# Optimization experiments

Hardware: AMD Instinct MI355X
Metric: run time of the kernel (lower is better)

## Reference

```python
import jax, jax.numpy as jnp
import numpy as np

N_NODES = 50000
N_EDGES = 800000
D_FEAT = 96


def setup_inputs() -> dict:
    key = jax.random.key(0)
    kx, ks, kd = jax.random.split(key, 3)
    x = jax.random.normal(kx, (N_NODES, D_FEAT), dtype=jnp.float32)
    src = jax.random.randint(ks, (N_EDGES,), 0, N_NODES, dtype=jnp.int64)
    dst = jax.random.randint(kd, (N_EDGES,), 0, N_NODES, dtype=jnp.int64)
    return {"x": x, "src": src, "dst": dst}


def reference(x, src, dst):
    n = x.shape[0]
    ones = jnp.ones(src.shape[0], dtype=x.dtype)
    # out-degree: edges leaving each node (src side)
    out_deg = jnp.clip(jax.ops.segment_sum(ones, src, num_segments=n), 1.0, None)
    # in-degree: edges arriving at each node (dst side)
    in_deg = jnp.clip(jax.ops.segment_sum(ones, dst, num_segments=n), 1.0, None)
    # pre-scale by out-degree^{-1/2}
    xs = x * (out_deg ** -0.5)[:, None]
    # copy_u + sum aggregation: sum messages from src into dst
    agg = jax.ops.segment_sum(xs[src], dst, num_segments=n)
    # post-scale by in-degree^{-1/2}
    return agg * (in_deg ** -0.5)[:, None]
```

## Files before the change

### kernel.cpp

```cpp
#include <hip/hip_runtime.h>


#define D_FEAT 96
#define CAP 64
#define PART_SHIFT 8
#define PNODES 256
#define NP_MAX 256
#define EPB 4096
#define OVF_CAP 8192

__device__ __forceinline__ unsigned short f2bf_rne(float f) {
    unsigned u = __float_as_uint(f);
    unsigned r = (u >> 16) & 1u;
    u += 0x7fffu + r;
    return (unsigned short)(u >> 16);
}


__global__ __launch_bounds__(256) void partition_kernel(
        const int* __restrict__ src, const int* __restrict__ dst,
        int n_edges, int np, int stride,
        int* __restrict__ pcur_d, int* __restrict__ pcur_s,
        unsigned* __restrict__ pbuf_d, unsigned short* __restrict__ pbuf_s,
        int* __restrict__ ctr,
        int* __restrict__ povf_d, int* __restrict__ sovf_d) {
    __shared__ int hcd[NP_MAX], hcs[NP_MAX];
    __shared__ int bd[NP_MAX], bs_[NP_MAX];
    __shared__ int od[NP_MAX], os_[NP_MAX];
    const int base = blockIdx.x * EPB;

    for (int i = threadIdx.x; i < NP_MAX; i += 256) {
        hcd[i] = 0; hcs[i] = 0; od[i] = 0; os_[i] = 0;
    }
    __syncthreads();

    unsigned v[16];
    #pragma unroll
    for (int k = 0; k < 16; ++k) {
        int i = base + (int)threadIdx.x + (k << 8);
        if (i < n_edges) {
            int s = src[i], d = dst[i];
            unsigned pv = (unsigned)d | ((unsigned)s << 16);
            v[k] = pv;
            atomicAdd(&hcd[d >> PART_SHIFT], 1);
            atomicAdd(&hcs[s >> PART_SHIFT], 1);
        }
    }
    __syncthreads();

    for (int p = threadIdx.x; p < np; p += 256) {
        int cd = hcd[p];
        bd[p] = cd ? atomicAdd(&pcur_d[p], cd) : 0;
        int cs = hcs[p];
        bs_[p] = cs ? atomicAdd(&pcur_s[p], cs) : 0;
    }
    __syncthreads();

    #pragma unroll
    for (int k = 0; k < 16; ++k) {
        int i = base + (int)threadIdx.x + (k << 8);
        if (i < n_edges) {
            unsigned pv = v[k];
            int d = (int)(pv & 0xffffu);
            int s = (int)(pv >> 16);
            int pd = d >> PART_SHIFT;
            int j = bd[pd] + atomicAdd(&od[pd], 1);
            if (j < stride) pbuf_d[(size_t)pd * stride + j] = pv;
            else { int k2 = atomicAdd(&ctr[1], 1); if (k2 < OVF_CAP) povf_d[k2] = (int)pv; }
            int ps = s >> PART_SHIFT;
            int j2 = bs_[ps] + atomicAdd(&os_[ps], 1);
            if (j2 < stride) pbuf_s[(size_t)ps * stride + j2] = (unsigned short)s;
            else { int k3 = atomicAdd(&ctr[2], 1); if (k3 < OVF_CAP) sovf_d[k3] = s; }
        }
    }
}


__global__ __launch_bounds__(256) void bin2_kernel(
        const unsigned* __restrict__ pbuf_d, const int* __restrict__ pcur_d,
        int stride, int n_nodes,
        int* __restrict__ cursor, unsigned short* __restrict__ slots,
        int* __restrict__ ctr, int* __restrict__ ovf_d) {
    __shared__ unsigned short lslots[PNODES * CAP];
    __shared__ int lcnt[PNODES];
    const int b = blockIdx.x;
    const int nbase = b << PART_SHIFT;
    const int nloc = min(PNODES, n_nodes - nbase);

    for (int i = threadIdx.x; i < PNODES; i += 256) lcnt[i] = 0;
    __syncthreads();

    int n = pcur_d[b]; if (n > stride) n = stride;
    for (int i = threadIdx.x; i < n; i += 256) {
        unsigned pv = pbuf_d[(size_t)b * stride + i];
        int dl = (int)(pv & 0xffu);
        int s  = (int)(pv >> 16);
        int pos = atomicAdd(&lcnt[dl], 1);
        if (pos < CAP) lslots[dl * CAP + pos] = (unsigned short)s;
        else { int k = atomicAdd(&ctr[0], 1); if (k < OVF_CAP) ovf_d[k] = (int)pv; }
    }
    __syncthreads();

    for (int i = threadIdx.x; i < nloc; i += 256) cursor[nbase + i] = lcnt[i];
    const unsigned* ls = (const unsigned*)lslots;
    unsigned* gs = (unsigned*)slots + (size_t)nbase * (CAP / 2);
    const int ncopy = nloc * (CAP / 2);
    for (int i = threadIdx.x; i < ncopy; i += 256) gs[i] = ls[i];
}


__global__ __launch_bounds__(256) void cnt2_kernel(
        const unsigned short* __restrict__ pbuf_s, const int* __restrict__ pcur_s,
        int stride, int n_nodes, int* __restrict__ out_cnt) {
    __shared__ int lcnt[PNODES];
    const int b = blockIdx.x;
    const int nbase = b << PART_SHIFT;
    const int nloc = min(PNODES, n_nodes - nbase);

    for (int i = threadIdx.x; i < PNODES; i += 256) lcnt[i] = 0;
    __syncthreads();

    int n = pcur_s[b]; if (n > stride) n = stride;
    for (int i = threadIdx.x; i < n; i += 256) {
        int s = (int)pbuf_s[(size_t)b * stride + i];
        atomicAdd(&lcnt[s & (PNODES - 1)], 1);
    }
    __syncthreads();

    for (int i = threadIdx.x; i < nloc; i += 256) out_cnt[nbase + i] = lcnt[i];
}

__global__ void fixup_kernel(int* __restrict__ ctr,
                             const int* __restrict__ povf_d,
                             const int* __restrict__ sovf_d,
                             int* __restrict__ ovf_d,
                             int* __restrict__ cursor,
                             int* __restrict__ out_cnt) {
    int np_ = ctr[1]; if (np_ > OVF_CAP) np_ = OVF_CAP;
    for (int i = threadIdx.x; i < np_; i += 256) {
        unsigned pv = (unsigned)povf_d[i];
        atomicAdd(&cursor[pv & 0xffffu], 1);
        int k = atomicAdd(&ctr[0], 1);
        if (k < OVF_CAP) ovf_d[k] = (int)pv;
    }
    int ns_ = ctr[2]; if (ns_ > OVF_CAP) ns_ = OVF_CAP;
    for (int i = threadIdx.x; i < ns_; i += 256)
        atomicAdd(&out_cnt[(unsigned)sovf_d[i]], 1);
}


__global__ void convert_kernel(const float* __restrict__ x,
                               const int* __restrict__ out_cnt,
                               unsigned* __restrict__ xs, int n_total) {
    int t = blockIdx.x * blockDim.x + threadIdx.x;
    if (t >= n_total) return;
    int node = t / 48;
    int j = t - node * 48;
    int c = out_cnt[node];
    float w = rsqrtf((float)(c < 1 ? 1 : c));
    float2 v = *(const float2*)(x + (size_t)node * D_FEAT + j * 2);
    unsigned lo = f2bf_rne(v.x * w);
    unsigned hi = f2bf_rne(v.y * w);
    xs[t] = lo | (hi << 16);
}

__global__ __launch_bounds__(256) void gather_kernel(
        const unsigned* __restrict__ xs,
        const unsigned short* __restrict__ slots,
        const int* __restrict__ cursor,
        float* __restrict__ out, int n_nodes) {
    int wid  = threadIdx.x >> 6;
    int lane = threadIdx.x & 63;
    int node = __builtin_amdgcn_readfirstlane(blockIdx.x * 4 + wid);
    if (node >= n_nodes) return;

    int cnt_all = __builtin_amdgcn_readfirstlane(cursor[node]);
    int cnt = cnt_all < CAP ? cnt_all : CAP;

    float2 acc = make_float2(0.f, 0.f);
    const bool act = lane < 48;

    if (cnt > 0) {
        int idx  = lane < cnt ? lane : cnt - 1;
        int sval = (int)slots[node * CAP + idx];

        int e = 0;
        for (; e + 8 <= cnt; e += 8) {
            int s0 = __builtin_amdgcn_readlane(sval, e);
            int s1 = __builtin_amdgcn_readlane(sval, e + 1);
            int s2 = __builtin_amdgcn_readlane(sval, e + 2);
            int s3 = __builtin_amdgcn_readlane(sval, e + 3);
            int s4 = __builtin_amdgcn_readlane(sval, e + 4);
            int s5 = __builtin_amdgcn_readlane(sval, e + 5);
            int s6 = __builtin_amdgcn_readlane(sval, e + 6);
            int s7 = __builtin_amdgcn_readlane(sval, e + 7);
            if (act) {
                unsigned u0 = xs[s0 * 48 + lane];
                unsigned u1 = xs[s1 * 48 + lane];
                unsigned u2 = xs[s2 * 48 + lane];
                unsigned u3 = xs[s3 * 48 + lane];
                unsigned u4 = xs[s4 * 48 + lane];
                unsigned u5 = xs[s5 * 48 + lane];
                unsigned u6 = xs[s6 * 48 + lane];
                unsigned u7 = xs[s7 * 48 + lane];
                acc.x += __uint_as_float(u0 << 16); acc.y += __uint_as_float(u0 & 0xffff0000u);
                acc.x += __uint_as_float(u1 << 16); acc.y += __uint_as_float(u1 & 0xffff0000u);
                acc.x += __uint_as_float(u2 << 16); acc.y += __uint_as_float(u2 & 0xffff0000u);
                acc.x += __uint_as_float(u3 << 16); acc.y += __uint_as_float(u3 & 0xffff0000u);
                acc.x += __uint_as_float(u4 << 16); acc.y += __uint_as_float(u4 & 0xffff0000u);
                acc.x += __uint_as_float(u5 << 16); acc.y += __uint_as_float(u5 & 0xffff0000u);
                acc.x += __uint_as_float(u6 << 16); acc.y += __uint_as_float(u6 & 0xffff0000u);
                acc.x += __uint_as_float(u7 << 16); acc.y += __uint_as_float(u7 & 0xffff0000u);
            }
        }
        for (; e + 4 <= cnt; e += 4) {
            int s0 = __builtin_amdgcn_readlane(sval, e);
            int s1 = __builtin_amdgcn_readlane(sval, e + 1);
            int s2 = __builtin_amdgcn_readlane(sval, e + 2);
            int s3 = __builtin_amdgcn_readlane(sval, e + 3);
            if (act) {
                unsigned u0 = xs[s0 * 48 + lane];
                unsigned u1 = xs[s1 * 48 + lane];
                unsigned u2 = xs[s2 * 48 + lane];
                unsigned u3 = xs[s3 * 48 + lane];
                acc.x += __uint_as_float(u0 << 16); acc.y += __uint_as_float(u0 & 0xffff0000u);
                acc.x += __uint_as_float(u1 << 16); acc.y += __uint_as_float(u1 & 0xffff0000u);
                acc.x += __uint_as_float(u2 << 16); acc.y += __uint_as_float(u2 & 0xffff0000u);
                acc.x += __uint_as_float(u3 << 16); acc.y += __uint_as_float(u3 & 0xffff0000u);
            }
        }
        for (; e < cnt; ++e) {
            int s0 = __builtin_amdgcn_readlane(sval, e);
            if (act) {
                unsigned u0 = xs[s0 * 48 + lane];
                acc.x += __uint_as_float(u0 << 16); acc.y += __uint_as_float(u0 & 0xffff0000u);
            }
        }
    }

    float sc = rsqrtf((float)(cnt_all < 1 ? 1 : cnt_all));
    if (act) {
        float2 r = make_float2(acc.x * sc, acc.y * sc);
        *(float2*)(out + (size_t)node * D_FEAT + lane * 2) = r;
    }
}

__global__ void overflow_kernel(const float* __restrict__ x,
                                const int* __restrict__ out_cnt,
                                const int* __restrict__ cursor,
                                const int* __restrict__ ctr,
                                const int* __restrict__ ovf_d,
                                float* __restrict__ out) {
    int count = ctr[0];
    if (count > OVF_CAP) count = OVF_CAP;
    int total = count * 24;
    int stride_t = gridDim.x * blockDim.x;
    for (int i = blockIdx.x * blockDim.x + threadIdx.x; i < total; i += stride_t) {
        int k = i / 24, c = i % 24;
        unsigned pv = (unsigned)ovf_d[k];
        int d = (int)(pv & 0xffffu);
        int s = (int)(pv >> 16);
        int co = out_cnt[s], ci = cursor[d];
        float w = rsqrtf((float)(co < 1 ? 1 : co)) * rsqrtf((float)(ci < 1 ? 1 : ci));
        const float4 v = *(const float4*)(x + (size_t)s * D_FEAT + c * 4);
        float* o = out + (size_t)d * D_FEAT + c * 4;
        unsafeAtomicAdd(o + 0, v.x * w);
        unsafeAtomicAdd(o + 1, v.y * w);
        unsafeAtomicAdd(o + 2, v.z * w);
        unsafeAtomicAdd(o + 3, v.w * w);
    }
}


__global__ void degree_kernel(const int* __restrict__ src,
                              const int* __restrict__ dst,
                              int* __restrict__ out_cnt,
                              int* __restrict__ in_cnt, int n_edges) {
    int i = blockIdx.x * blockDim.x + threadIdx.x;
    if (i < n_edges) {
        atomicAdd(&out_cnt[src[i]], 1);
        atomicAdd(&in_cnt[dst[i]], 1);
    }
}

__global__ void scale_kernel(float* __restrict__ osc, float* __restrict__ isc, int n) {
    int i = blockIdx.x * blockDim.x + threadIdx.x;
    if (i < n) {
        int c0 = ((const int*)osc)[i];
        int c1 = ((const int*)isc)[i];
        osc[i] = rsqrtf((float)(c0 < 1 ? 1 : c0));
        isc[i] = rsqrtf((float)(c1 < 1 ? 1 : c1));
    }
}

__global__ void scatter_kernel(const float* __restrict__ x,
                               const int* __restrict__ src,
                               const int* __restrict__ dst,
                               const float* __restrict__ osc,
                               const float* __restrict__ isc,
                               float* __restrict__ out, int n_edges) {
    int idx = blockIdx.x * blockDim.x + threadIdx.x;
    int e = idx / 24, c = idx % 24;
    if (e >= n_edges) return;
    int s = src[e], d = dst[e];
    float w = osc[s] * isc[d];
    const float4 v = *(const float4*)(x + (size_t)s * D_FEAT + c * 4);
    float* o = out + (size_t)d * D_FEAT + c * 4;
    unsafeAtomicAdd(o + 0, v.x * w);
    unsafeAtomicAdd(o + 1, v.y * w);
    unsafeAtomicAdd(o + 2, v.z * w);
    unsafeAtomicAdd(o + 3, v.w * w);
}


extern "C" void kernel_launch(void* const* d_in, const int* in_sizes, int n_in,
                              void* d_out, int out_size, void* d_ws, size_t ws_size,
                              hipStream_t stream) {
    const float* x  = (const float*)d_in[0];
    const int* src  = (const int*)d_in[1];
    const int* dst  = (const int*)d_in[2];
    float* out      = (float*)d_out;

    const int n_edges = in_sizes[1];
    const int n_nodes = in_sizes[0] / D_FEAT;

    const int np = (n_nodes + PNODES - 1) / PNODES;
    const int avg = n_edges / (np > 0 ? np : 1);
    const int stride = avg + avg / 4 + 1024;

    const size_t pbuf_words  = (size_t)np * stride;
    const size_t pbufs_words = (pbuf_words + 1) / 2;

    int* pcur_d  = (int*)d_ws;
    int* pcur_s  = pcur_d + 256;
    int* ctr     = pcur_d + 512;
    int* ovf_d   = pcur_d + 1024;
    int* povf_d  = ovf_d + OVF_CAP;
    int* sovf_d  = povf_d + OVF_CAP;
    int* out_cnt = sovf_d + OVF_CAP;
    int* cursor  = out_cnt + 65536;
    unsigned* pbuf_dst = (unsigned*)(cursor + 65536);
    unsigned short* pbuf_src = (unsigned short*)(pbuf_dst + pbuf_words);
    unsigned* xs = pbuf_dst + pbuf_words + pbufs_words;
    unsigned short* slots = (unsigned short*)(xs + (size_t)n_nodes * 48);

    const size_t needed = ((size_t)1024 + 3 * OVF_CAP + 2 * 65536 + pbuf_words +
                           pbufs_words + (size_t)n_nodes * 48 +
                           (size_t)n_nodes * (CAP / 2)) * 4;

    if (ws_size >= needed && n_nodes <= 65536 && np <= NP_MAX) {
        hipMemsetAsync(d_ws, 0, 1024 * sizeof(int), stream);

        partition_kernel<<<(n_edges + EPB - 1) / EPB, 256, 0, stream>>>(
            src, dst, n_edges, np, stride, pcur_d, pcur_s,
            pbuf_dst, pbuf_src, ctr, povf_d, sovf_d);

        bin2_kernel<<<np, 256, 0, stream>>>(
            pbuf_dst, pcur_d, stride, n_nodes, cursor, slots, ctr, ovf_d);

        cnt2_kernel<<<np, 256, 0, stream>>>(
            pbuf_src, pcur_s, stride, n_nodes, out_cnt);

        fixup_kernel<<<1, 256, 0, stream>>>(
            ctr, povf_d, sovf_d, ovf_d, cursor, out_cnt);

        const int n_pairs = n_nodes * 48;
        convert_kernel<<<(n_pairs + 255) / 256, 256, 0, stream>>>(
            x, out_cnt, xs, n_pairs);

        gather_kernel<<<(n_nodes + 3) / 4, 256, 0, stream>>>(
            xs, slots, cursor, out, n_nodes);

        overflow_kernel<<<32, 256, 0, stream>>>(
            x, out_cnt, cursor, ctr, ovf_d, out);
    } else {
        float* osc = (float*)d_ws;
        float* isc = osc + 65536;
        hipMemsetAsync(d_ws, 0, 2 * 65536 * sizeof(int), stream);
        hipMemsetAsync(d_out, 0, (size_t)out_size * sizeof(float), stream);
        degree_kernel<<<(n_edges + 255) / 256, 256, 0, stream>>>(
            src, dst, (int*)osc, (int*)isc, n_edges);
        scale_kernel<<<(n_nodes + 255) / 256, 256, 0, stream>>>(osc, isc, n_nodes);
        const int total = n_edges * 24;
        scatter_kernel<<<(total + 255) / 256, 256, 0, stream>>>(
            x, src, dst, osc, isc, out, n_edges);
    }
}
```

Before: 143.4 us.

## Split bf16 feature table into three 32-column planes and gather each in separate pass

The scaled bf16 node table is now written as three planes of 16 words (32 features) per node, and the gather runs three times, one plane per pass. Each pass touches only about a third of the table, so its working set is more likely to stay in L2/MALL. Within a pass the wave splits into 4 sub-groups of 16 lanes that each take a different edge, then reduce with cross-lane xor shuffles and write with nontemporal stores. The cost is three kernel launches, re-reading slots and cursors three times, 64-byte gathers per edge, and the extra shuffle reduction.

```diff
diff --git a/kernel.cpp b/kernel.cpp
--- a/kernel.cpp
+++ b/kernel.cpp
@@ -151,8 +151,9 @@
 
 __global__ void convert_kernel(const float* __restrict__ x,
                                const int* __restrict__ out_cnt,
-                               unsigned* __restrict__ xs, int n_total) {
+                               unsigned* __restrict__ xs, int n_nodes) {
     int t = blockIdx.x * blockDim.x + threadIdx.x;
+    int n_total = n_nodes * 48;
     if (t >= n_total) return;
     int node = t / 48;
     int j = t - node * 48;
@@ -161,14 +162,17 @@
     float2 v = *(const float2*)(x + (size_t)node * D_FEAT + j * 2);
     unsigned lo = f2bf_rne(v.x * w);
     unsigned hi = f2bf_rne(v.y * w);
-    xs[t] = lo | (hi << 16);
-}
-
-__global__ __launch_bounds__(256) void gather_kernel(
-        const unsigned* __restrict__ xs,
+    int p = j >> 4, fj = j & 15;
+    xs[((size_t)p * n_nodes + node) * 16 + fj] = lo | (hi << 16);
+}
+
+
+__global__ __launch_bounds__(256) void gather3_kernel(
+        const unsigned* __restrict__ xsp,
         const unsigned short* __restrict__ slots,
         const int* __restrict__ cursor,
-        float* __restrict__ out, int n_nodes) {
+        float* __restrict__ outp,
+        int n_nodes) {
     int wid  = threadIdx.x >> 6;
     int lane = threadIdx.x & 63;
     int node = __builtin_amdgcn_readfirstlane(blockIdx.x * 4 + wid);
@@ -177,71 +181,33 @@
     int cnt_all = __builtin_amdgcn_readfirstlane(cursor[node]);
     int cnt = cnt_all < CAP ? cnt_all : CAP;
 
-    float2 acc = make_float2(0.f, 0.f);
-    const bool act = lane < 48;
-
+    const int sub = lane >> 4;
+    const int fj  = lane & 15;
+
+    float accx = 0.f, accy = 0.f;
     if (cnt > 0) {
         int idx  = lane < cnt ? lane : cnt - 1;
-        int sval = (int)slots[node * CAP + idx];
-
-        int e = 0;
-        for (; e + 8 <= cnt; e += 8) {
-            int s0 = __builtin_amdgcn_readlane(sval, e);
-            int s1 = __builtin_amdgcn_readlane(sval, e + 1);
-            int s2 = __builtin_amdgcn_readlane(sval, e + 2);
-            int s3 = __builtin_amdgcn_readlane(sval, e + 3);
-            int s4 = __builtin_amdgcn_readlane(sval, e + 4);
-            int s5 = __builtin_amdgcn_readlane(sval, e + 5);
-            int s6 = __builtin_amdgcn_readlane(sval, e + 6);
-            int s7 = __builtin_amdgcn_readlane(sval, e + 7);
-            if (act) {
-                unsigned u0 = xs[s0 * 48 + lane];
-                unsigned u1 = xs[s1 * 48 + lane];
-                unsigned u2 = xs[s2 * 48 + lane];
-                unsigned u3 = xs[s3 * 48 + lane];
-                unsigned u4 = xs[s4 * 48 + lane];
-                unsigned u5 = xs[s5 * 48 + lane];
-                unsigned u6 = xs[s6 * 48 + lane];
-                unsigned u7 = xs[s7 * 48 + lane];
-                acc.x += __uint_as_float(u0 << 16); acc.y += __uint_as_float(u0 & 0xffff0000u);
-                acc.x += __uint_as_float(u1 << 16); acc.y += __uint_as_float(u1 & 0xffff0000u);
-                acc.x += __uint_as_float(u2 << 16); acc.y += __uint_as_float(u2 & 0xffff0000u);
-                acc.x += __uint_as_float(u3 << 16); acc.y += __uint_as_float(u3 & 0xffff0000u);
-                acc.x += __uint_as_float(u4 << 16); acc.y += __uint_as_float(u4 & 0xffff0000u);
-                acc.x += __uint_as_float(u5 << 16); acc.y += __uint_as_float(u5 & 0xffff0000u);
-                acc.x += __uint_as_float(u6 << 16); acc.y += __uint_as_float(u6 & 0xffff0000u);
-                acc.x += __uint_as_float(u7 << 16); acc.y += __uint_as_float(u7 & 0xffff0000u);
+        int sval = (int)__builtin_nontemporal_load(&slots[node * CAP + idx]);
+
+        for (int e = 0; e < cnt; e += 4) {
+            int ee = e + sub;
+            bool valid = ee < cnt;
+            int s = __shfl(sval, valid ? ee : cnt - 1, 64);
+            unsigned u = xsp[(size_t)s * 16 + fj];
+            if (valid) {
+                accx += __uint_as_float(u << 16);
+                accy += __uint_as_float(u & 0xffff0000u);
             }
         }
-        for (; e + 4 <= cnt; e += 4) {
-            int s0 = __builtin_amdgcn_readlane(sval, e);
-            int s1 = __builtin_amdgcn_readlane(sval, e + 1);
-            int s2 = __builtin_amdgcn_readlane(sval, e + 2);
-            int s3 = __builtin_amdgcn_readlane(sval, e + 3);
-            if (act) {
-                unsigned u0 = xs[s0 * 48 + lane];
-                unsigned u1 = xs[s1 * 48 + lane];
-                unsigned u2 = xs[s2 * 48 + lane];
-                unsigned u3 = xs[s3 * 48 + lane];
-                acc.x += __uint_as_float(u0 << 16); acc.y += __uint_as_float(u0 & 0xffff0000u);
-                acc.x += __uint_as_float(u1 << 16); acc.y += __uint_as_float(u1 & 0xffff0000u);
-                acc.x += __uint_as_float(u2 << 16); acc.y += __uint_as_float(u2 & 0xffff0000u);
-                acc.x += __uint_as_float(u3 << 16); acc.y += __uint_as_float(u3 & 0xffff0000u);
-            }
-        }
-        for (; e < cnt; ++e) {
-            int s0 = __builtin_amdgcn_readlane(sval, e);
-            if (act) {
-                unsigned u0 = xs[s0 * 48 + lane];
-                acc.x += __uint_as_float(u0 << 16); acc.y += __uint_as_float(u0 & 0xffff0000u);
-            }
-        }
+        accx += __shfl_xor(accx, 32, 64); accy += __shfl_xor(accy, 32, 64);
+        accx += __shfl_xor(accx, 16, 64); accy += __shfl_xor(accy, 16, 64);
     }
 
     float sc = rsqrtf((float)(cnt_all < 1 ? 1 : cnt_all));
-    if (act) {
-        float2 r = make_float2(acc.x * sc, acc.y * sc);
-        *(float2*)(out + (size_t)node * D_FEAT + lane * 2) = r;
+    if (sub == 0) {
+        float* op = outp + (size_t)node * D_FEAT + fj * 2;
+        __builtin_nontemporal_store(accx * sc, op);
+        __builtin_nontemporal_store(accy * sc, op + 1);
     }
 }
 
@@ -349,7 +315,7 @@
                            (size_t)n_nodes * (CAP / 2)) * 4;
 
     if (ws_size >= needed && n_nodes <= 65536 && np <= NP_MAX) {
-        hipMemsetAsync(d_ws, 0, 1024 * sizeof(int), stream);
+        (void)hipMemsetAsync(d_ws, 0, 1024 * sizeof(int), stream);
 
         partition_kernel<<<(n_edges + EPB - 1) / EPB, 256, 0, stream>>>(
             src, dst, n_edges, np, stride, pcur_d, pcur_s,
@@ -366,18 +332,22 @@
 
         const int n_pairs = n_nodes * 48;
         convert_kernel<<<(n_pairs + 255) / 256, 256, 0, stream>>>(
-            x, out_cnt, xs, n_pairs);
-
-        gather_kernel<<<(n_nodes + 3) / 4, 256, 0, stream>>>(
-            xs, slots, cursor, out, n_nodes);
+            x, out_cnt, xs, n_nodes);
+
+        const int gblk = (n_nodes + 3) / 4;
+        for (int p = 0; p < 3; ++p) {
+            gather3_kernel<<<gblk, 256, 0, stream>>>(
+                xs + (size_t)p * n_nodes * 16, slots, cursor,
+                out + 32 * p, n_nodes);
+        }
 
         overflow_kernel<<<32, 256, 0, stream>>>(
             x, out_cnt, cursor, ctr, ovf_d, out);
     } else {
         float* osc = (float*)d_ws;
         float* isc = osc + 65536;
-        hipMemsetAsync(d_ws, 0, 2 * 65536 * sizeof(int), stream);
-        hipMemsetAsync(d_out, 0, (size_t)out_size * sizeof(float), stream);
+        (void)hipMemsetAsync(d_ws, 0, 2 * 65536 * sizeof(int), stream);
+        (void)hipMemsetAsync(d_out, 0, (size_t)out_size * sizeof(float), stream);
         degree_kernel<<<(n_edges + 255) / 256, 256, 0, stream>>>(
             src, dst, (int*)osc, (int*)isc, n_edges);
         scale_kernel<<<(n_nodes + 255) / 256, 256, 0, stream>>>(osc, isc, n_nodes);
```

After: 177.9 us. 24.1% more time.
